# Performance work log

Measured on AMD Instinct MI355X. Metric: run time of the kernel, lower is better.

## Reference

```python
import jax, jax.numpy as jnp
import numpy as np

B, C, IN, OUT = 256, 919, 400, 100

def setup_inputs() -> dict:
    key = jax.random.key(0)
    k1, k2 = jax.random.split(key)
    inputs = jax.random.normal(k1, (B, C, IN), dtype=jnp.float32)
    # glorot-style scaling for kernel
    kernel = jax.random.normal(k2, (1, C, IN, OUT), dtype=jnp.float32) * (1.0 / np.sqrt(IN))
    bias = jnp.zeros((1, C, OUT), dtype=jnp.float32)
    return {"inputs": inputs, "kernel": kernel, "bias": bias}

def reference(inputs, kernel, bias):
    # Original: broadcast (B,C,IN,1) * (1,C,IN,OUT), reduce over IN, add bias.
    # Equivalent fused form: per-category batched GEMM.
    # inputs: (B, C, IN); kernel: (1, C, IN, OUT) -> out: (B, C, OUT)
    out = jnp.einsum('bci,cio->bco', inputs, kernel[0])
    out = out + bias  # (1, C, OUT) broadcasts over batch
    return out  # activation is None (linear)
```

## Files before the change

kernel.cpp:

```cpp
#include <hip/hip_runtime.h>
#include <stdint.h>

#define BATCH 256
#define NCAT  919
#define KDIM  400
#define NDIM  100
#define BK    32
#define NSTEP 13
#define NPAD  112
#define LROW  40
#define ABUF  (BATCH * LROW)
#define WBUF  (NPAD * LROW)
#define BUFSZ (ABUF + WBUF)

typedef float  f32x4  __attribute__((ext_vector_type(4)));
typedef __bf16 bf16x8 __attribute__((ext_vector_type(8)));
typedef unsigned short u16;
typedef u16    u16x8  __attribute__((ext_vector_type(8)));

__device__ __forceinline__ u16 f2bf(float f) {
  union { float f; uint32_t u; } v; v.f = f;
  uint32_t r = v.u + 0x7fffu + ((v.u >> 16) & 1u);
  return (u16)(r >> 16);
}

__global__ void __launch_bounds__(512, 4)
cat_dense(const float* __restrict__ in, const float* __restrict__ wt,
          const float* __restrict__ bias, float* __restrict__ out)
{
  __shared__ u16 lds[2 * BUFSZ];

  const int c    = blockIdx.x;
  const int tid  = threadIdx.x;
  const int lane = tid & 63;
  const int wave = tid >> 6;

  const int a_row = tid >> 2;
  const int a_kq  = (tid & 3) * 8;
  const bool w_act = tid < 400;
  const int w_kp  = tid / 25;
  const int w_nq  = (tid - w_kp * 25) * 4;

  const float* gA = in + (size_t)c * KDIM;
  const float* gW = wt + (size_t)c * (KDIM * NDIM);

  f32x4 areg[2][2];
  f32x4 wreg[2];

  auto load_step = [&](int t) {
    const int kb = t * BK;
    #pragma unroll
    for (int i = 0; i < 2; ++i) {
      const int row = a_row + i * 128;
      if (kb + a_kq < KDIM) {
        const float* p = gA + (size_t)row * (NCAT * KDIM) + kb + a_kq;
        areg[i][0] = *(const f32x4*)p;
        areg[i][1] = *(const f32x4*)(p + 4);
      } else {
        areg[i][0] = {0.f,0.f,0.f,0.f};
        areg[i][1] = {0.f,0.f,0.f,0.f};
      }
    }
    const int k0 = kb + 2 * w_kp;
    if (w_act && k0 < KDIM) {
      const float* p = gW + (size_t)k0 * NDIM + w_nq;
      wreg[0] = *(const f32x4*)p;
      wreg[1] = *(const f32x4*)(p + NDIM);
    } else {
      wreg[0] = {0.f,0.f,0.f,0.f};
      wreg[1] = {0.f,0.f,0.f,0.f};
    }
  };

  auto write_step = [&](int buf) {
    u16* L = &lds[buf * BUFSZ];
    #pragma unroll
    for (int i = 0; i < 2; ++i) {
      const int row = a_row + i * 128;
      u16x8 v;
      #pragma unroll
      for (int j = 0; j < 4; ++j) {
        v[j]     = f2bf(areg[i][0][j]);
        v[4 + j] = f2bf(areg[i][1][j]);
      }
      *(u16x8*)&L[row * LROW + a_kq] = v;
    }
    if (w_act) {
      u16* Lw = L + ABUF;
      #pragma unroll
      for (int j = 0; j < 4; ++j) {
        uint32_t pk = (uint32_t)f2bf(wreg[0][j]) | ((uint32_t)f2bf(wreg[1][j]) << 16);
        *(uint32_t*)&Lw[(w_nq + j) * LROW + 2 * w_kp] = pk;
      }
    }
  };

  f32x4 acc[2][7];
  #pragma unroll
  for (int m = 0; m < 2; ++m)
    #pragma unroll
    for (int n = 0; n < 7; ++n)
      acc[m][n] = {0.f,0.f,0.f,0.f};

  const int rl = lane & 15;
  const int kg = (lane >> 4) * 8;

  auto compute = [&](int buf) {
    const u16* L  = &lds[buf * BUFSZ];
    const u16* Lw = L + ABUF;
    bf16x8 a0 = *(const bf16x8*)&L[(wave * 32 +      rl) * LROW + kg];
    bf16x8 a1 = *(const bf16x8*)&L[(wave * 32 + 16 + rl) * LROW + kg];
    #pragma unroll
    for (int n = 0; n < 7; ++n) {
      bf16x8 b = *(const bf16x8*)&Lw[(n * 16 + rl) * LROW + kg];
      acc[0][n] = __builtin_amdgcn_mfma_f32_16x16x32_bf16(a0, b, acc[0][n], 0, 0, 0);
      acc[1][n] = __builtin_amdgcn_mfma_f32_16x16x32_bf16(a1, b, acc[1][n], 0, 0, 0);
    }
  };

  load_step(0);
  write_step(0);
  __syncthreads();

  for (int t = 0; t < NSTEP; ++t) {
    const int buf = t & 1;
    if (t + 1 < NSTEP) load_step(t + 1);
    compute(buf);
    if (t + 1 < NSTEP) {
      __syncthreads();
      write_step(buf ^ 1);
      __syncthreads();
    }
  }

  const float* gB = bias + (size_t)c * NDIM;
  float* gO = out + (size_t)c * NDIM;
  #pragma unroll
  for (int n = 0; n < 7; ++n) {
    const int col = n * 16 + rl;
    if (col < NDIM) {
      const float bv = gB[col];
      #pragma unroll
      for (int m = 0; m < 2; ++m) {
        const int r0 = wave * 32 + m * 16 + (lane >> 4) * 4;
        #pragma unroll
        for (int j = 0; j < 4; ++j) {
          gO[(size_t)(r0 + j) * (NCAT * NDIM) + col] = acc[m][n][j] + bv;
        }
      }
    }
  }
}

extern "C" void kernel_launch(void* const* d_in, const int* in_sizes, int n_in,
                              void* d_out, int out_size, void* d_ws, size_t ws_size,
                              hipStream_t stream) {
  const float* in   = (const float*)d_in[0];
  const float* wt   = (const float*)d_in[1];
  const float* bias = (const float*)d_in[2];
  float* o          = (float*)d_out;
  cat_dense<<<dim3(NCAT), dim3(512), 0, stream>>>(in, wt, bias, o);
}
```

Before: 160.1 us.

## Load A fragments directly to registers and triple-buffer weight tile in LDS

Activations are now read from global memory straight into each lane's MFMA fragment registers and converted to bf16 there, so the A tile no longer goes through shared memory. Only the weight tile is staged in LDS, with a triple buffer and register double-buffering that allow one barrier per K step instead of two. The loop is fully unrolled, and the software bf16 rounding is replaced by native casts. In exchange, the per-lane global loads are less coalesced (32-byte chunks per row) and register pressure rises.

```diff
diff --git a/kernel.cpp b/kernel.cpp
--- a/kernel.cpp
+++ b/kernel.cpp
@@ -1,7 +1,6 @@
 #include <hip/hip_runtime.h>
 #include <stdint.h>
 
-#define BATCH 256
 #define NCAT  919
 #define KDIM  400
 #define NDIM  100
@@ -9,128 +8,112 @@
 #define NSTEP 13
 #define NPAD  112
 #define LROW  40
-#define ABUF  (BATCH * LROW)
 #define WBUF  (NPAD * LROW)
-#define BUFSZ (ABUF + WBUF)
 
 typedef float  f32x4  __attribute__((ext_vector_type(4)));
 typedef __bf16 bf16x8 __attribute__((ext_vector_type(8)));
-typedef unsigned short u16;
-typedef u16    u16x8  __attribute__((ext_vector_type(8)));
-
-__device__ __forceinline__ u16 f2bf(float f) {
-  union { float f; uint32_t u; } v; v.f = f;
-  uint32_t r = v.u + 0x7fffu + ((v.u >> 16) & 1u);
-  return (u16)(r >> 16);
-}
+typedef __bf16 bf16x2 __attribute__((ext_vector_type(2)));
 
 __global__ void __launch_bounds__(512, 4)
 cat_dense(const float* __restrict__ in, const float* __restrict__ wt,
           const float* __restrict__ bias, float* __restrict__ out)
 {
-  __shared__ u16 lds[2 * BUFSZ];
+  __shared__ __bf16 wlds[3 * WBUF];
 
   const int c    = blockIdx.x;
   const int tid  = threadIdx.x;
   const int lane = tid & 63;
   const int wave = tid >> 6;
 
-  const int a_row = tid >> 2;
-  const int a_kq  = (tid & 3) * 8;
   const bool w_act = tid < 400;
-  const int w_kp  = tid / 25;
-  const int w_nq  = (tid - w_kp * 25) * 4;
+  const int  w_kp  = tid / 25;
+  const int  w_nq  = (tid - w_kp * 25) * 4;
+  const float* gW  = wt + (size_t)c * (KDIM * NDIM);
 
-  const float* gA = in + (size_t)c * KDIM;
-  const float* gW = wt + (size_t)c * (KDIM * NDIM);
+  const int rl = lane & 15;
+  const int kg = (lane >> 4) * 8;
+  const size_t rstride = (size_t)NCAT * KDIM;
+  const float* gA0 = in + (size_t)c * KDIM + (size_t)(wave * 32 + rl) * rstride;
+  const float* gA1 = gA0 + (size_t)16 * rstride;
 
-  f32x4 areg[2][2];
-  f32x4 wreg[2];
-
-  auto load_step = [&](int t) {
-    const int kb = t * BK;
-    #pragma unroll
-    for (int i = 0; i < 2; ++i) {
-      const int row = a_row + i * 128;
-      if (kb + a_kq < KDIM) {
-        const float* p = gA + (size_t)row * (NCAT * KDIM) + kb + a_kq;
-        areg[i][0] = *(const f32x4*)p;
-        areg[i][1] = *(const f32x4*)(p + 4);
-      } else {
-        areg[i][0] = {0.f,0.f,0.f,0.f};
-        areg[i][1] = {0.f,0.f,0.f,0.f};
-      }
-    }
-    const int k0 = kb + 2 * w_kp;
-    if (w_act && k0 < KDIM) {
-      const float* p = gW + (size_t)k0 * NDIM + w_nq;
-      wreg[0] = *(const f32x4*)p;
-      wreg[1] = *(const f32x4*)(p + NDIM);
-    } else {
-      wreg[0] = {0.f,0.f,0.f,0.f};
-      wreg[1] = {0.f,0.f,0.f,0.f};
-    }
-  };
-
-  auto write_step = [&](int buf) {
-    u16* L = &lds[buf * BUFSZ];
-    #pragma unroll
-    for (int i = 0; i < 2; ++i) {
-      const int row = a_row + i * 128;
-      u16x8 v;
-      #pragma unroll
-      for (int j = 0; j < 4; ++j) {
-        v[j]     = f2bf(areg[i][0][j]);
-        v[4 + j] = f2bf(areg[i][1][j]);
-      }
-      *(u16x8*)&L[row * LROW + a_kq] = v;
-    }
-    if (w_act) {
-      u16* Lw = L + ABUF;
-      #pragma unroll
-      for (int j = 0; j < 4; ++j) {
-        uint32_t pk = (uint32_t)f2bf(wreg[0][j]) | ((uint32_t)f2bf(wreg[1][j]) << 16);
-        *(uint32_t*)&Lw[(w_nq + j) * LROW + 2 * w_kp] = pk;
-      }
-    }
-  };
-
+  f32x4 wreg[2][2];
+  f32x4 areg[2][2][2];
   f32x4 acc[2][7];
   #pragma unroll
   for (int m = 0; m < 2; ++m)
     #pragma unroll
-    for (int n = 0; n < 7; ++n)
-      acc[m][n] = {0.f,0.f,0.f,0.f};
+    for (int n = 0; n < 7; ++n) acc[m][n] = f32x4{0.f, 0.f, 0.f, 0.f};
 
-  const int rl = lane & 15;
-  const int kg = (lane >> 4) * 8;
+#define LOADW(T, S) do {                                                  \
+    const int k0_ = (T) * BK + 2 * w_kp;                                  \
+    if (w_act && k0_ < KDIM) {                                            \
+      const float* p_ = gW + (size_t)k0_ * NDIM + w_nq;                   \
+      wreg[S][0] = *(const f32x4*)p_;                                     \
+      wreg[S][1] = *(const f32x4*)(p_ + NDIM);                            \
+    } else {                                                              \
+      wreg[S][0] = f32x4{0.f,0.f,0.f,0.f};                                \
+      wreg[S][1] = f32x4{0.f,0.f,0.f,0.f};                                \
+    }                                                                     \
+  } while (0)
 
-  auto compute = [&](int buf) {
-    const u16* L  = &lds[buf * BUFSZ];
-    const u16* Lw = L + ABUF;
-    bf16x8 a0 = *(const bf16x8*)&L[(wave * 32 +      rl) * LROW + kg];
-    bf16x8 a1 = *(const bf16x8*)&L[(wave * 32 + 16 + rl) * LROW + kg];
+#define WRITEW(S, BUF) do {                                               \
+    if (w_act) {                                                          \
+      __bf16* Lw_ = &wlds[(BUF) * WBUF];                                  \
+      _Pragma("unroll")                                                   \
+      for (int j_ = 0; j_ < 4; ++j_) {                                    \
+        bf16x2 pk_ = { (__bf16)wreg[S][0][j_], (__bf16)wreg[S][1][j_] };  \
+        *(bf16x2*)&Lw_[(w_nq + j_) * LROW + 2 * w_kp] = pk_;              \
+      }                                                                   \
+    }                                                                     \
+  } while (0)
+
+#define LOADA(T, PP) do {                                                 \
+    const int kb_ = (T) * BK + kg;                                        \
+    if (kb_ < KDIM) {        \
+      areg[PP][0][0] = *(const f32x4*)(gA0 + kb_);                        \
+      areg[PP][0][1] = *(const f32x4*)(gA0 + kb_ + 4);                    \
+      areg[PP][1][0] = *(const f32x4*)(gA1 + kb_);                        \
+      areg[PP][1][1] = *(const f32x4*)(gA1 + kb_ + 4);                    \
+    } else {                                                              \
+      areg[PP][0][0] = f32x4{0.f,0.f,0.f,0.f};                            \
+      areg[PP][0][1] = f32x4{0.f,0.f,0.f,0.f};                            \
+      areg[PP][1][0] = f32x4{0.f,0.f,0.f,0.f};                            \
+      areg[PP][1][1] = f32x4{0.f,0.f,0.f,0.f};                            \
+    }                                                                     \
+  } while (0)
+
+  LOADW(0, 0);
+  LOADA(0, 0);
+  WRITEW(0, 0);
+  LOADW(1, 1);
+  asm volatile("s_waitcnt lgkmcnt(0)" ::: "memory");
+  __builtin_amdgcn_s_barrier();
+
+  #pragma unroll
+  for (int t = 0; t < NSTEP; ++t) {
+    const int buf = t % 3;
+    const int pp  = t & 1;
+    if (t + 1 < NSTEP) LOADA(t + 1, pp ^ 1);
+    if (t + 2 < NSTEP) LOADW(t + 2, t & 1);
+    if (t + 1 < NSTEP) WRITEW((t + 1) & 1, (t + 1) % 3);
+
+    bf16x8 a0, a1;
+    #pragma unroll
+    for (int j = 0; j < 4; ++j) {
+      a0[j]     = (__bf16)areg[pp][0][0][j];
+      a0[4 + j] = (__bf16)areg[pp][0][1][j];
+      a1[j]     = (__bf16)areg[pp][1][0][j];
+      a1[4 + j] = (__bf16)areg[pp][1][1][j];
+    }
+    const __bf16* Lw = &wlds[buf * WBUF];
     #pragma unroll
     for (int n = 0; n < 7; ++n) {
       bf16x8 b = *(const bf16x8*)&Lw[(n * 16 + rl) * LROW + kg];
       acc[0][n] = __builtin_amdgcn_mfma_f32_16x16x32_bf16(a0, b, acc[0][n], 0, 0, 0);
       acc[1][n] = __builtin_amdgcn_mfma_f32_16x16x32_bf16(a1, b, acc[1][n], 0, 0, 0);
     }
-  };
-
-  load_step(0);
-  write_step(0);
-  __syncthreads();
-
-  for (int t = 0; t < NSTEP; ++t) {
-    const int buf = t & 1;
-    if (t + 1 < NSTEP) load_step(t + 1);
-    compute(buf);
-    if (t + 1 < NSTEP) {
-      __syncthreads();
-      write_step(buf ^ 1);
-      __syncthreads();
-    }
+    asm volatile("s_waitcnt lgkmcnt(0)" ::: "memory");
+    __builtin_amdgcn_s_barrier();
   }
 
   const float* gB = bias + (size_t)c * NDIM;
```

Result: slower. 181.1 us (+13.2%).
